# Kernel tuning notes

Measured on AMD Instinct MI355X. Metric: run time of the kernel, lower is better.

The kernel has to match this reference:

```python
import jax, jax.numpy as jnp
import numpy as np

EPS = 1e-5
NUM_GROUPS = 32


def group_norm(x, num_groups=NUM_GROUPS, eps=EPS):
    # x: [B, C, H, W]; normalize over (C//G, H, W) per group, no affine
    B, C, H, W = x.shape
    xg = x.reshape(B, num_groups, C // num_groups, H, W)
    mean = xg.mean(axis=(2, 3, 4), keepdims=True)
    var = xg.var(axis=(2, 3, 4), keepdims=True)
    xg = (xg - mean) * jax.lax.rsqrt(var + eps)
    return xg.reshape(B, C, H, W)


def nin(x, W, b):
    # 1x1 dense projection over channel dim: [B,C,H,W] x [C,O] -> [B,O,H,W]
    return jnp.einsum('bchw,co->bohw', x, W) + b[None, :, None, None]


def setup_inputs() -> dict:
    key = jax.random.key(0)
    ks = jax.random.split(key, 9)
    B, C, H, W_ = 32, 512, 32, 32
    s = 1.0 / np.sqrt(C)
    return {
        'x': jax.random.normal(ks[0], (B, C, H, W_), jnp.float32),
        'Wq': jax.random.normal(ks[1], (C, C), jnp.float32) * s,
        'bq': jnp.zeros((C,), jnp.float32),
        'Wk': jax.random.normal(ks[2], (C, C), jnp.float32) * s,
        'bk': jnp.zeros((C,), jnp.float32),
        'Wv': jax.random.normal(ks[3], (C, C), jnp.float32) * s,
        'bv': jnp.zeros((C,), jnp.float32),
        'Wn': jax.random.normal(ks[4], (C, C), jnp.float32) * (0.05 * s),
        'bn': jnp.zeros((C,), jnp.float32),
    }


def reference(x, Wq, bq, Wk, bk, Wv, bv, Wn, bn):
    B, C, H, W_ = x.shape
    h = group_norm(x)
    q = nin(h, Wq, bq)
    k = nin(h, Wk, bk)
    v = nin(h, Wv, bv)
    scale = jnp.asarray(C, x.dtype) ** -0.5
    # full spatial attention: [B, H, W, H', W']
    w = jnp.einsum('bchw,bcHW->bhwHW', q, k) * scale
    w = w.reshape(B, H, W_, H * W_)
    w = jax.nn.softmax(w, axis=-1)
    w = w.reshape(B, H, W_, H, W_)
    h = jnp.einsum('bhwHW,bcHW->bchw', w, v)
    h = nin(h, Wn, bn)
    return x + h
```

## Files before the change

kernel.cpp:

```cpp
#include <hip/hip_runtime.h>
#include <cstdint>

#define B_   32
#define C_   512
#define N_   1024
#define G_   32
#define CG_  16

typedef unsigned short u16;
typedef unsigned char u8;
typedef unsigned long long u64;

static constexpr float kEps = 1e-5f;
static constexpr float kLog2Scale = 0.06375871752987579f;

using f32x4  = __attribute__((ext_vector_type(4))) float;
using short8 = __attribute__((ext_vector_type(8))) short;
using i64x2  = __attribute__((ext_vector_type(2))) long long;

__device__ __forceinline__ u16 f2bf(float f) {
  uint32_t u = __builtin_bit_cast(uint32_t, f);
  u += 0x7fffu + ((u >> 16) & 1u);
  return (u16)(u >> 16);
}
__device__ __forceinline__ float bf2f(u16 h) {
  return __builtin_bit_cast(float, (uint32_t)h << 16);
}
__device__ __forceinline__ int pk4_fp8(float a, float b, float c, float d) {
  int w = __builtin_amdgcn_cvt_pk_fp8_f32(a, b, 0, false);
  w = __builtin_amdgcn_cvt_pk_fp8_f32(c, d, w, true);
  return w;
}
__device__ __forceinline__ int f8pos(int k) {
  const int c8 = (k >> 3) & 7;
  return (k & ~63) + ((c8 & 3) << 4) + ((c8 >> 2) << 3) + (k & 4);
}

__device__ __forceinline__ void gload16(const void* g, void* lds) {
  __builtin_amdgcn_global_load_lds(
      (__attribute__((address_space(1))) void*)(uintptr_t)g,
      (__attribute__((address_space(3))) void*)(uint32_t)(uintptr_t)lds,
      16, 0, 0);
}

__device__ __forceinline__ uint3 remap_xcd() {
  const int gx = gridDim.x, gy = gridDim.y, gz = gridDim.z;
  const int nwg = gx * gy * gz;
  const int lin = blockIdx.x + gx * (blockIdx.y + gy * blockIdx.z);
  const int q = nwg >> 3, r = nwg & 7;
  const int xcd = lin & 7, pos = lin >> 3;
  int nid = (xcd < r ? xcd * (q + 1) : r * (q + 1) + (xcd - r) * q) + pos;
  uint3 o;
  o.x = nid % gx; nid /= gx;
  o.y = nid % gy; o.z = nid / gy;
  return o;
}

__global__ __launch_bounds__(256) void wcvt_kernel(
    const float* __restrict__ Wq, const float* __restrict__ Wk,
    const float* __restrict__ Wv, u16* __restrict__ Wab, u16* __restrict__ Wbb) {
  const int idx = blockIdx.x * 256 + threadIdx.x;
  const int src = idx >> 16;
  const int e = (idx & 65535) * 4;
  const float* W = (src == 0) ? Wq : (src == 1) ? Wk : Wv;
  u16* D = (src == 0) ? Wab : (src == 1) ? Wbb : (Wab + 262144);
  const float4 v = *(const float4*)(W + e);
  ushort4 st;
  st.x = f2bf(v.x); st.y = f2bf(v.y); st.z = f2bf(v.z); st.w = f2bf(v.w);
  *(ushort4*)(D + e) = st;
}

__global__ __launch_bounds__(256) void wtr_kernel(
    const float* __restrict__ Wn, u16* __restrict__ Wtn) {
  __shared__ float tile[64][65];
  const int c0 = blockIdx.y * 64, o0 = blockIdx.x * 64;
  const int tx = threadIdx.x & 15, ty = threadIdx.x >> 4;
#pragma unroll
  for (int rr = 0; rr < 64; rr += 16) {
    const int c = c0 + ty + rr;
    const float4 v = *(const float4*)(Wn + (size_t)c * 512 + o0 + tx * 4);
    tile[ty + rr][tx * 4 + 0] = v.x;
    tile[ty + rr][tx * 4 + 1] = v.y;
    tile[ty + rr][tx * 4 + 2] = v.z;
    tile[ty + rr][tx * 4 + 3] = v.w;
  }
  __syncthreads();
#pragma unroll
  for (int rr = 0; rr < 64; rr += 16) {
    const int o = o0 + ty + rr;
    ushort4 st;
    st.x = f2bf(tile[tx * 4 + 0][ty + rr]);
    st.y = f2bf(tile[tx * 4 + 1][ty + rr]);
    st.z = f2bf(tile[tx * 4 + 2][ty + rr]);
    st.w = f2bf(tile[tx * 4 + 3][ty + rr]);
    *(ushort4*)(Wtn + (size_t)o * 512 + c0 + tx * 4) = st;
  }
}

__global__ __launch_bounds__(512) void biask_kernel(
    const float* __restrict__ Wk, const float* __restrict__ bq,
    const float* __restrict__ Wn, const float* __restrict__ bv,
    const float* __restrict__ bn, float* __restrict__ wkbq,
    float* __restrict__ bvn) {
  const int t = threadIdx.x;
  if (blockIdx.x == 0) {
    float s = 0.f;
    const float* row = Wk + (size_t)t * 512;
    for (int o = 0; o < 512; ++o) s += row[o] * bq[o];
    wkbq[t] = s;
  } else {
    float s = 0.f;
    for (int c = 0; c < 512; ++c) s += bv[c] * Wn[(size_t)c * 512 + t];
    bvn[t] = s + bn[t];
  }
}

__global__ __launch_bounds__(256) void gn_fused(const float* __restrict__ x,
                                                u8* __restrict__ Hn8,
                                                u8* __restrict__ HnT8) {
  __shared__ u16 lds2[16 * 1032];
  __shared__ float red[10];
  const int bg = blockIdx.x, b = bg >> 5, g = bg & 31;
  const int t = threadIdx.x;
  const float4* p4 = (const float4*)(x + (size_t)bg * 16384);
  float s = 0.f, s2 = 0.f;
  for (int i = t; i < 4096; i += 256) {
    const float4 v = p4[i];
    const int e = i * 4, ic = e >> 10, n = e & 1023;
    ushort4 sv;
    sv.x = f2bf(v.x); sv.y = f2bf(v.y); sv.z = f2bf(v.z); sv.w = f2bf(v.w);
    *(ushort4*)(lds2 + ic * 1032 + n) = sv;
    s  += v.x + v.y + v.z + v.w;
    s2 += v.x * v.x + v.y * v.y + v.z * v.z + v.w * v.w;
  }
#pragma unroll
  for (int o = 32; o; o >>= 1) { s += __shfl_xor(s, o); s2 += __shfl_xor(s2, o); }
  const int lane = t & 63, w = t >> 6;
  if (lane == 0) { red[w] = s; red[4 + w] = s2; }
  __syncthreads();
  if (t == 0) {
    s  = red[0] + red[1] + red[2] + red[3];
    s2 = red[4] + red[5] + red[6] + red[7];
    const float inv = 1.0f / 16384.0f;
    const float mean = s * inv;
    const float var  = s2 * inv - mean * mean;
    red[8] = mean;
    red[9] = rsqrtf(var + kEps);
  }
  __syncthreads();
  const float mean = red[8], rstd = red[9];
#pragma unroll
  for (int r = 0; r < 4; ++r) {
    const int n = t + 256 * r;
    float vals[16];
#pragma unroll
    for (int ic = 0; ic < 16; ++ic)
      vals[ic] = (bf2f(lds2[ic * 1032 + n]) - mean) * rstd;
    const u64 lo = (u64)(uint32_t)pk4_fp8(vals[0], vals[1], vals[2], vals[3]) |
                   ((u64)(uint32_t)pk4_fp8(vals[4], vals[5], vals[6], vals[7]) << 32);
    const u64 hi = (u64)(uint32_t)pk4_fp8(vals[8], vals[9], vals[10], vals[11]) |
                   ((u64)(uint32_t)pk4_fp8(vals[12], vals[13], vals[14], vals[15]) << 32);
    u8* rb = Hn8 + ((size_t)(b * N_ + n)) * C_;
    *(u64*)(rb + f8pos(g * 16))     = lo;
    *(u64*)(rb + f8pos(g * 16 + 8)) = hi;
  }
  const int nb = t * 4;
#pragma unroll
  for (int ic = 0; ic < 16; ++ic) {
    const ushort4 hv = *(const ushort4*)(lds2 + ic * 1032 + nb);
    const int wv = pk4_fp8((bf2f(hv.x) - mean) * rstd, (bf2f(hv.y) - mean) * rstd,
                           (bf2f(hv.z) - mean) * rstd, (bf2f(hv.w) - mean) * rstd);
    *(int*)(HnT8 + ((size_t)(b * C_ + g * 16 + ic)) * N_ + f8pos(nb)) = wv;
  }
}

__global__ __launch_bounds__(256) void gemm_w128(
    const u16* __restrict__ Ab, const u16* __restrict__ Bb, u8* __restrict__ Ob) {
  __shared__ u16 Alds[128 * 64];
  __shared__ u16 Blds[128 * 64];
  const int p = blockIdx.z;
  const u16* A = Ab + (size_t)p * 262144;
  const u16* B = Bb + (size_t)p * 262144;
  u8* O = Ob + (size_t)p * 262144;
  const int m0 = blockIdx.y * 128, n0 = blockIdx.x * 128;
  const int tid = threadIdx.x, lane = tid & 63, wid = tid >> 6;
  const int wm = wid >> 1, wn = wid & 1;
  const int sr = lane >> 3, scb = (lane & 7) ^ sr;
  const u16* Ag = A + (size_t)(m0 + wid * 32 + sr) * 512 + scb * 8;
  const u16* Bg = B + (size_t)(n0 + wid * 32 + sr) * 512 + scb * 8;
  char* Al = (char*)Alds + wid * 4096;
  char* Bl = (char*)Blds + wid * 4096;
  const int arow = lane & 15, g4 = lane >> 4, rx = lane & 7;
  f32x4 acc[4][4] = {};
  for (int k = 0; k < 512; k += 64) {
#pragma unroll
    for (int g = 0; g < 4; ++g) {
      gload16(Ag + k + g * (8 * 512), Al + g * 1024);
      gload16(Bg + k + g * (8 * 512), Bl + g * 1024);
    }
    __syncthreads();
#pragma unroll
    for (int kk = 0; kk < 2; ++kk) {
      const int pc = ((kk * 4 + g4) ^ rx) * 16;
      short8 a[4], b[4];
#pragma unroll
      for (int i = 0; i < 4; ++i)
        a[i] = *(const short8*)((const char*)Alds + (wm * 64 + i * 16 + arow) * 128 + pc);
#pragma unroll
      for (int j = 0; j < 4; ++j)
        b[j] = *(const short8*)((const char*)Blds + (wn * 64 + j * 16 + arow) * 128 + pc);
#pragma unroll
      for (int i = 0; i < 4; ++i)
#pragma unroll
        for (int j = 0; j < 4; ++j)
          acc[i][j] = __builtin_amdgcn_mfma_f32_16x16x32_bf16(a[i], b[j], acc[i][j], 0, 0, 0);
    }
    __syncthreads();
  }
#pragma unroll
  for (int i = 0; i < 4; ++i) {
    const int rowg = m0 + wm * 64 + i * 16 + ((lane >> 4) * 4);
#pragma unroll
    for (int j = 0; j < 4; ++j) {
      const int colg = n0 + wn * 64 + j * 16 + (lane & 15);
      const f32x4 v = acc[i][j];
      *(int*)(O + (size_t)colg * 512 + f8pos(rowg)) =
          pk4_fp8(v[0], v[1], v[2], v[3]);
    }
  }
}

#define LDA8_(D, BASE, MH)                                                      \
  _Pragma("unroll")                                                             \
  for (int i_ = 0; i_ < 4; ++i_) {                                              \
    const int rr_ = wm * 128 + (MH) * 64 + i_ * 16 + arow;                      \
    D[i_] = *(const i64x2*)((BASE) + rr_ * 64 +                                 \
                            ((g4 ^ ((rr_ >> 1) & 3)) << 4));                    \
  }
#define LDB8_(D, BASE)                                                          \
  _Pragma("unroll")                                                             \
  for (int j_ = 0; j_ < 4; ++j_) {                                              \
    const int rr_ = wn * 64 + j_ * 16 + arow;                                   \
    D[j_] = *(const i64x2*)((BASE) + rr_ * 64 +                                 \
                            ((g4 ^ ((rr_ >> 1) & 3)) << 4));                    \
  }
#define MM8_(ACC, AA, BB, H)                                                    \
  __builtin_amdgcn_s_setprio(1);                                                \
  _Pragma("unroll")                                                             \
  for (int i_ = 0; i_ < 4; ++i_)                                                \
    _Pragma("unroll")                                                           \
    for (int j_ = 0; j_ < 4; ++j_)                                              \
      ACC[i_][j_] = __builtin_amdgcn_mfma_f32_16x16x32_fp8_fp8(                 \
          AA[i_][H], BB[j_][H], ACC[i_][j_], 0, 0, 0);                          \
  __builtin_amdgcn_s_setprio(0);

__device__ __forceinline__ void gemm_core256_f8(
    const u8* __restrict__ A, const u8* __restrict__ B,
    int Ktot, int m0, int n0,
    char* Alds, char* Blds, f32x4 acc0[4][4], f32x4 acc1[4][4]) {
  const int tid = threadIdx.x, lane = tid & 63, wid = tid >> 6;
  const int wm = wid >> 2, wn = wid & 3;
  const int rl = lane >> 2;
  const int c16 = (lane & 3) ^ ((lane >> 3) & 3);
  const u8* Ag = A + (size_t)(m0 + wid * 32 + rl) * Ktot + c16 * 16;
  const u8* Bg = B + (size_t)(n0 + wid * 32 + rl) * Ktot + c16 * 16;
  char* Al = Alds + wid * 2048;
  char* Bl = Blds + wid * 2048;
  const long long r16 = (long long)16 * Ktot;
  const int arow = lane & 15, g4 = lane >> 4;
  const int nt = Ktot >> 6;

#pragma unroll
  for (int g = 0; g < 2; ++g) {
    gload16(Ag + g * r16, Al + g * 1024);
    gload16(Bg + g * r16, Bl + g * 1024);
  }
  asm volatile("s_waitcnt vmcnt(0)" ::: "memory");
  __builtin_amdgcn_s_barrier();
  i64x2 aX[4], aY[4], bX[4];
  LDA8_(aX, Alds, 0);

  for (int t = 0; t < nt; ++t) {
    const int cur = t & 1;
    const char* Ab = Alds + cur * 16384;
    const char* Bb = Blds + cur * 16384;
    const char* An = Alds + (cur ^ 1) * 16384;
    char* Aln = Al + (cur ^ 1) * 16384;
    char* Bln = Bl + (cur ^ 1) * 16384;
    const bool nx = (t + 1 < nt);
    const long long ko = (long long)(t + 1) * 64;

    if (nx) {
#pragma unroll
      for (int g = 0; g < 2; ++g) gload16(Bg + ko + g * r16, Bln + g * 1024);
    }
    LDB8_(bX, Bb);
    LDA8_(aY, Ab, 1);
    asm volatile("s_waitcnt lgkmcnt(4)" ::: "memory");
    __builtin_amdgcn_sched_barrier(0);
    __builtin_amdgcn_s_barrier();
    MM8_(acc0, aX, bX, 0);

    if (nx) {
#pragma unroll
      for (int g = 0; g < 2; ++g) gload16(Ag + ko + g * r16, Aln + g * 1024);
    }
    asm volatile("s_waitcnt lgkmcnt(0)" ::: "memory");
    __builtin_amdgcn_sched_barrier(0);
    __builtin_amdgcn_s_barrier();
    MM8_(acc1, aY, bX, 0);

    __builtin_amdgcn_sched_barrier(0);
    __builtin_amdgcn_s_barrier();
    MM8_(acc0, aX, bX, 1);

    if (nx) {
      asm volatile("s_waitcnt vmcnt(0)" ::: "memory");
    }
    __builtin_amdgcn_sched_barrier(0);
    __builtin_amdgcn_s_barrier();
    if (nx) {
      LDA8_(aX, An, 0);
    }
    MM8_(acc1, aY, bX, 1);
  }
}

__device__ __forceinline__ void copy_out_tile(const char* SH, u8* O, int LDC,
                                              int m0, int n0) {
  const int tid = threadIdx.x;
#pragma unroll
  for (int it = 0; it < 8; ++it) {
    const int flat = it * 8192 + tid * 16;
    const int row = flat >> 8, col = flat & 255;
    *(int4*)(O + (size_t)(n0 + row) * LDC + m0 + col) =
        *(const int4*)(SH + row * 256 + (col ^ ((row & 15) << 4)));
  }
}

__global__ __launch_bounds__(512, 2) void gemm_hwq_f8(
    const u8* __restrict__ Wqk8, const u8* __restrict__ Hn8,
    const float* __restrict__ wkbq, u8* __restrict__ HWq8) {
  __shared__ char SH[4 * 256 * 64];
  const uint3 bid = remap_xcd();
  const int z = bid.z;
  const u8* B = Hn8 + (size_t)z * ((size_t)N_ * C_);
  u8* O = HWq8 + (size_t)z * ((size_t)N_ * C_);
  const int m0 = bid.y * 256, n0 = bid.x * 256;
  f32x4 acc0[4][4] = {};
  f32x4 acc1[4][4] = {};
  gemm_core256_f8(Wqk8, B, 512, m0, n0, SH, SH + 32768, acc0, acc1);

  const int lane = threadIdx.x & 63, wid = threadIdx.x >> 6;
  const int wm = wid >> 2, wn = wid & 3;
  __syncthreads();
#pragma unroll
  for (int i = 0; i < 8; ++i) {
    const int ml = wm * 128 + i * 16 + ((lane >> 4) * 4);
    const float4 bv = *(const float4*)(wkbq + m0 + ml);
    const int fp = f8pos(ml);
#pragma unroll
    for (int j = 0; j < 4; ++j) {
      const int nl = wn * 64 + j * 16 + (lane & 15);
      const f32x4 v = (i < 4) ? acc0[i][j] : acc1[i - 4][j];
      *(int*)(SH + nl * 256 + (fp ^ ((nl & 15) << 4))) =
          pk4_fp8(v[0] + bv.x, v[1] + bv.y, v[2] + bv.z, v[3] + bv.w);
    }
  }
  __syncthreads();
  copy_out_tile(SH, O, 512, m0, n0);
}

__global__ __launch_bounds__(512, 2) void gemm_s_f8(
    const u8* __restrict__ Hn8, const u8* __restrict__ HWq8,
    u8* __restrict__ P8, float* __restrict__ Psum) {
  __shared__ char SH[4 * 256 * 64];
  const uint3 bid = remap_xcd();
  const int z = bid.z;
  const u8* A = Hn8  + (size_t)z * ((size_t)N_ * C_);
  const u8* B = HWq8 + (size_t)z * ((size_t)N_ * C_);
  u8*       O = P8   + (size_t)z * ((size_t)N_ * N_);
  const int m0 = bid.y * 256, n0 = bid.x * 256;
  f32x4 acc0[4][4] = {};
  f32x4 acc1[4][4] = {};
  gemm_core256_f8(A, B, 512, m0, n0, SH, SH + 32768, acc0, acc1);

  const int lane = threadIdx.x & 63, wid = threadIdx.x >> 6;
  const int wm = wid >> 2, wn = wid & 3;
  float psum[4] = {0.f, 0.f, 0.f, 0.f};
  __syncthreads();
#pragma unroll
  for (int i = 0; i < 8; ++i) {
    const int ml = wm * 128 + i * 16 + ((lane >> 4) * 4);
    const int fp = f8pos(ml);
#pragma unroll
    for (int j = 0; j < 4; ++j) {
      const int nl = wn * 64 + j * 16 + (lane & 15);
      const f32x4 v = (i < 4) ? acc0[i][j] : acc1[i - 4][j];
      const float p0 = __builtin_exp2f(v[0] * kLog2Scale) * 0.0625f;
      const float p1 = __builtin_exp2f(v[1] * kLog2Scale) * 0.0625f;
      const float p2 = __builtin_exp2f(v[2] * kLog2Scale) * 0.0625f;
      const float p3 = __builtin_exp2f(v[3] * kLog2Scale) * 0.0625f;
      psum[j] += (p0 + p1) + (p2 + p3);
      *(int*)(SH + nl * 256 + (fp ^ ((nl & 15) << 4))) = pk4_fp8(p0, p1, p2, p3);
    }
  }
  const int slot = (m0 >> 7) + wm;
  float* Ps = Psum + ((size_t)z * 8 + slot) * N_;
#pragma unroll
  for (int j = 0; j < 4; ++j) {
    float r = psum[j];
    r += __shfl_xor(r, 16);
    r += __shfl_xor(r, 32);
    if (lane < 16) Ps[n0 + wn * 64 + j * 16 + lane] = r;
  }
  __syncthreads();
  copy_out_tile(SH, O, 1024, m0, n0);
}

__global__ __launch_bounds__(512, 1) void gemm_pvf_f8(
    const u8* __restrict__ HnT8, const u8* __restrict__ P8,
    const float* __restrict__ Psum, const u8* __restrict__ Wvn8,
    const float* __restrict__ x, const float* __restrict__ bvn,
    float* __restrict__ Out) {
  __shared__ char SH[147456];
  char* Abuf = SH;
  char* Bbuf = SH + 65536;
  char* H2   = SH + 81920;
  const uint3 bid = remap_xcd();
  const int z = bid.z;
  const u8* A = HnT8 + (size_t)z * ((size_t)N_ * C_);
  const u8* B = P8   + (size_t)z * ((size_t)N_ * N_);
  const int n0 = bid.x * 128;
  const int tid = threadIdx.x, lane = tid & 63, wid = tid >> 6;
  const int wm = wid >> 1, wn = wid & 1;
  const int rl = lane >> 2;
  const int c16 = (lane & 3) ^ ((lane >> 3) & 3);
  const u8* Ag = A + (size_t)(wid * 64 + rl) * 1024 + c16 * 16;
  const u8* Bg = B + (size_t)(n0 + wid * 16 + rl) * 1024 + c16 * 16;
  const int arow = lane & 15, g4 = lane >> 4;
  f32x4 acc0[4][4] = {};
  f32x4 acc1[4][4] = {};

#pragma unroll
  for (int g = 0; g < 4; ++g)
    gload16(Ag + (size_t)g * (16 * 1024), Abuf + wid * 4096 + g * 1024);
  gload16(Bg, Bbuf + wid * 1024);
  asm volatile("s_waitcnt vmcnt(0)" ::: "memory");
  __builtin_amdgcn_s_barrier();
  i64x2 aX[4], aY[4], bX[4];
  LDA8_(aX, Abuf, 0);

  for (int t = 0; t < 16; ++t) {
    const int cur = t & 1;
    const char* Ab = Abuf + cur * 32768;
    const char* Bb = Bbuf + cur * 8192;
    const char* An = Abuf + (cur ^ 1) * 32768;
    const bool nx = (t + 1 < 16);
    const long long ko = (long long)(t + 1) * 64;

    if (nx) gload16(Bg + ko, Bbuf + (cur ^ 1) * 8192 + wid * 1024);
    LDB8_(bX, Bb);
    LDA8_(aY, Ab, 1);
    asm volatile("s_waitcnt lgkmcnt(4)" ::: "memory");
    __builtin_amdgcn_sched_barrier(0);
    __builtin_amdgcn_s_barrier();
    MM8_(acc0, aX, bX, 0);

    if (nx) {
#pragma unroll
      for (int g = 0; g < 4; ++g)
        gload16(Ag + ko + (size_t)g * (16 * 1024),
                Abuf + (cur ^ 1) * 32768 + wid * 4096 + g * 1024);
    }
    asm volatile("s_waitcnt lgkmcnt(0)" ::: "memory");
    __builtin_amdgcn_sched_barrier(0);
    __builtin_amdgcn_s_barrier();
    MM8_(acc1, aY, bX, 0);

    __builtin_amdgcn_sched_barrier(0);
    __builtin_amdgcn_s_barrier();
    MM8_(acc0, aX, bX, 1);

    if (nx) {
      asm volatile("s_waitcnt vmcnt(0)" ::: "memory");
    }
    __builtin_amdgcn_sched_barrier(0);
    __builtin_amdgcn_s_barrier();
    if (nx) {
      LDA8_(aX, An, 0);
    }
    MM8_(acc1, aY, bX, 1);
  }

  const float* Ps = Psum + (size_t)z * 8 * N_;
  float inv[4];
#pragma unroll
  for (int j = 0; j < 4; ++j) {
    const int ng = n0 + wn * 64 + j * 16 + (lane & 15);
    float s = 0.f;
#pragma unroll
    for (int k = 0; k < 8; ++k) s += Ps[k * N_ + ng];
    inv[j] = 1.0f / s;
  }
#pragma unroll
  for (int i = 0; i < 8; ++i) {
    const int c = wm * 128 + i * 16 + ((lane >> 4) * 4);
    const int fp = f8pos(c);
    const int ck = fp >> 4, sub = fp & 15;
#pragma unroll
    for (int j = 0; j < 4; ++j) {
      const int nl = wn * 64 + j * 16 + (lane & 15);
      const f32x4 v = (i < 4) ? acc0[i][j] : acc1[i - 4][j];
      *(int*)(H2 + nl * 512 + ((ck ^ (nl & 15)) << 4) + sub) =
          pk4_fp8(v[0] * inv[j], v[1] * inv[j], v[2] * inv[j], v[3] * inv[j]);
    }
  }
  __syncthreads();

  const int wmf = wid >> 2, wnf = wid & 3;
  f32x4 acc2[4][8] = {};
#pragma unroll
  for (int t = 0; t < 8; ++t) {
    i64x2 a2[4], b2[8];
#pragma unroll
    for (int i = 0; i < 4; ++i) {
      const int rn = wmf * 64 + i * 16 + arow;
      a2[i] = *(const i64x2*)(H2 + rn * 512 + (((t * 4 + g4) ^ (rn & 15)) << 4));
    }
#pragma unroll
    for (int j = 0; j < 8; ++j) {
      const int ro = wnf * 128 + j * 16 + arow;
      b2[j] = *(const i64x2*)(Wvn8 + (size_t)ro * 512 + t * 64 + g4 * 16);
    }
#pragma unroll
    for (int i = 0; i < 4; ++i)
#pragma unroll
      for (int j = 0; j < 8; ++j)
        acc2[i][j] = __builtin_amdgcn_mfma_f32_16x16x32_fp8_fp8(
            a2[i][0], b2[j][0], acc2[i][j], 0, 0, 0);
#pragma unroll
    for (int i = 0; i < 4; ++i)
#pragma unroll
      for (int j = 0; j < 8; ++j)
        acc2[i][j] = __builtin_amdgcn_mfma_f32_16x16x32_fp8_fp8(
            a2[i][1], b2[j][1], acc2[i][j], 0, 0, 0);
  }

  const float* xb = x + (size_t)z * ((size_t)C_ * N_);
  float* Ob = Out + (size_t)z * ((size_t)C_ * N_);
#pragma unroll
  for (int i = 0; i < 4; ++i) {
    const int rown = n0 + wmf * 64 + i * 16 + ((lane >> 4) * 4);
#pragma unroll
    for (int j = 0; j < 8; ++j) {
      const int colo = wnf * 128 + j * 16 + (lane & 15);
      const float bc = bvn[colo];
      const size_t off = (size_t)colo * N_ + rown;
      const float4 xv = *(const float4*)(xb + off);
      const f32x4 v = acc2[i][j];
      float4 ov;
      ov.x = xv.x + v[0] + bc;
      ov.y = xv.y + v[1] + bc;
      ov.z = xv.z + v[2] + bc;
      ov.w = xv.w + v[3] + bc;
      *(float4*)(Ob + off) = ov;
    }
  }
}

__global__ void sentinel_kernel(float* out, int n, float v) {
  const int i = blockIdx.x * blockDim.x + threadIdx.x;
  if (i < n) out[i] = v;
}

extern "C" void kernel_launch(void* const* d_in, const int* in_sizes, int n_in,
                              void* d_out, int out_size, void* d_ws, size_t ws_size,
                              hipStream_t stream) {
  const float* x  = (const float*)d_in[0];
  const float* Wq = (const float*)d_in[1];
  const float* bq = (const float*)d_in[2];
  const float* Wk = (const float*)d_in[3];
  const float* Wv = (const float*)d_in[5];
  const float* bv = (const float*)d_in[6];
  const float* Wn = (const float*)d_in[7];
  const float* bn = (const float*)d_in[8];
  float* out = (float*)d_out;

  char* ws = (char*)d_ws;
  size_t off = 0;
  u16* Wab = (u16*)(ws + off); off += (size_t)2 * 262144 * 2;
  u16* Wbb = (u16*)(ws + off); off += (size_t)2 * 262144 * 2;
  u8*  W8  = (u8*)(ws + off);  off += (size_t)2 * 262144;
  float* wkbq = (float*)(ws + off); off += 512 * 4;
  float* bvn  = (float*)(ws + off); off += 512 * 4;
  const size_t bnc = (size_t)B_ * N_ * C_;
  u8* Hn8  = (u8*)(ws + off); off += bnc;
  u8* HnT8 = (u8*)(ws + off); off += bnc;
  u8* HWq8 = (u8*)(ws + off); off += bnc;
  u8* P8   = (u8*)(ws + off); off += (size_t)B_ * N_ * N_;
  float* Psum = (float*)(ws + off); off += (size_t)B_ * 8 * N_ * 4;

  if (ws_size < off) {
    const float v = 1.0e6f + (float)(ws_size >> 20);
    sentinel_kernel<<<(out_size + 255) / 256, 256, 0, stream>>>(out, out_size, v);
    return;
  }

  wcvt_kernel<<<768, 256, 0, stream>>>(Wq, Wk, Wv, Wab, Wbb);
  wtr_kernel<<<dim3(8, 8), 256, 0, stream>>>(Wn, Wbb + 262144);
  biask_kernel<<<2, 512, 0, stream>>>(Wk, bq, Wn, bv, bn, wkbq, bvn);
  gn_fused<<<B_ * G_, 256, 0, stream>>>(x, Hn8, HnT8);
  gemm_w128<<<dim3(4, 4, 2), 256, 0, stream>>>(Wab, Wbb, W8);
  gemm_hwq_f8<<<dim3(4, 2, B_), 512, 0, stream>>>(W8, Hn8, wkbq, HWq8);
  gemm_s_f8<<<dim3(4, 4, B_), 512, 0, stream>>>(Hn8, HWq8, P8, Psum);
  gemm_pvf_f8<<<dim3(8, 1, B_), 512, 0, stream>>>(HnT8, P8, Psum, W8 + 262144, x, bvn, out);
}
```

Measured before the change: 192.2 us.

## Halve PV tile width in fused PV+output kernel to double grid and occupancy

Shrinks the gemm_pvf_f8 column tile from 128 to 64 query positions, doubling the grid to 512 blocks. LDS drops from 144KB to 72KB by aliasing the H2 staging buffer onto the A buffer (with an added barrier), and launch bounds allow more blocks per CU. Only four waves now load the smaller B tile. The aim is better CU fill and latency hiding, at the cost of re-reading the full HnT8 panel and Wvn weights twice as often per batch.

```diff
diff --git a/kernel.cpp b/kernel.cpp
--- a/kernel.cpp
+++ b/kernel.cpp
@@ -244,12 +244,28 @@
     D[j_] = *(const i64x2*)((BASE) + rr_ * 64 +                                 \
                             ((g4 ^ ((rr_ >> 1) & 3)) << 4));                    \
   }
+#define LDB8J2_(D, BASE)                                                        \
+  _Pragma("unroll")                                                             \
+  for (int j_ = 0; j_ < 2; ++j_) {                                              \
+    const int rr_ = wn * 32 + j_ * 16 + arow;                                   \
+    D[j_] = *(const i64x2*)((BASE) + rr_ * 64 +                                 \
+                            ((g4 ^ ((rr_ >> 1) & 3)) << 4));                    \
+  }
 #define MM8_(ACC, AA, BB, H)                                                    \
   __builtin_amdgcn_s_setprio(1);                                                \
   _Pragma("unroll")                                                             \
   for (int i_ = 0; i_ < 4; ++i_)                                                \
     _Pragma("unroll")                                                           \
     for (int j_ = 0; j_ < 4; ++j_)                                              \
+      ACC[i_][j_] = __builtin_amdgcn_mfma_f32_16x16x32_fp8_fp8(                 \
+          AA[i_][H], BB[j_][H], ACC[i_][j_], 0, 0, 0);                          \
+  __builtin_amdgcn_s_setprio(0);
+#define MM8J2_(ACC, AA, BB, H)                                                  \
+  __builtin_amdgcn_s_setprio(1);                                                \
+  _Pragma("unroll")                                                             \
+  for (int i_ = 0; i_ < 4; ++i_)                                                \
+    _Pragma("unroll")                                                           \
+    for (int j_ = 0; j_ < 2; ++j_)                                              \
       ACC[i_][j_] = __builtin_amdgcn_mfma_f32_16x16x32_fp8_fp8(                 \
           AA[i_][H], BB[j_][H], ACC[i_][j_], 0, 0, 0);                          \
   __builtin_amdgcn_s_setprio(0);
@@ -418,20 +434,20 @@
   copy_out_tile(SH, O, 1024, m0, n0);
 }
 
-__global__ __launch_bounds__(512, 1) void gemm_pvf_f8(
+__global__ __launch_bounds__(512, 4) void gemm_pvf_f8(
     const u8* __restrict__ HnT8, const u8* __restrict__ P8,
     const float* __restrict__ Psum, const u8* __restrict__ Wvn8,
     const float* __restrict__ x, const float* __restrict__ bvn,
     float* __restrict__ Out) {
-  __shared__ char SH[147456];
+  __shared__ char SH[73728];
   char* Abuf = SH;
   char* Bbuf = SH + 65536;
-  char* H2   = SH + 81920;
+  char* H2   = SH;
   const uint3 bid = remap_xcd();
   const int z = bid.z;
   const u8* A = HnT8 + (size_t)z * ((size_t)N_ * C_);
   const u8* B = P8   + (size_t)z * ((size_t)N_ * N_);
-  const int n0 = bid.x * 128;
+  const int n0 = bid.x * 64;
   const int tid = threadIdx.x, lane = tid & 63, wid = tid >> 6;
   const int wm = wid >> 1, wn = wid & 1;
   const int rl = lane >> 2;
@@ -439,33 +455,33 @@
   const u8* Ag = A + (size_t)(wid * 64 + rl) * 1024 + c16 * 16;
   const u8* Bg = B + (size_t)(n0 + wid * 16 + rl) * 1024 + c16 * 16;
   const int arow = lane & 15, g4 = lane >> 4;
-  f32x4 acc0[4][4] = {};
-  f32x4 acc1[4][4] = {};
+  f32x4 acc0[4][2] = {};
+  f32x4 acc1[4][2] = {};
 
 #pragma unroll
   for (int g = 0; g < 4; ++g)
     gload16(Ag + (size_t)g * (16 * 1024), Abuf + wid * 4096 + g * 1024);
-  gload16(Bg, Bbuf + wid * 1024);
+  if (wid < 4) gload16(Bg, Bbuf + wid * 1024);
   asm volatile("s_waitcnt vmcnt(0)" ::: "memory");
   __builtin_amdgcn_s_barrier();
-  i64x2 aX[4], aY[4], bX[4];
+  i64x2 aX[4], aY[4], bX[2];
   LDA8_(aX, Abuf, 0);
 
   for (int t = 0; t < 16; ++t) {
     const int cur = t & 1;
     const char* Ab = Abuf + cur * 32768;
-    const char* Bb = Bbuf + cur * 8192;
+    const char* Bb = Bbuf + cur * 4096;
     const char* An = Abuf + (cur ^ 1) * 32768;
     const bool nx = (t + 1 < 16);
     const long long ko = (long long)(t + 1) * 64;
 
-    if (nx) gload16(Bg + ko, Bbuf + (cur ^ 1) * 8192 + wid * 1024);
-    LDB8_(bX, Bb);
+    if (nx && wid < 4) gload16(Bg + ko, Bbuf + (cur ^ 1) * 4096 + wid * 1024);
+    LDB8J2_(bX, Bb);
     LDA8_(aY, Ab, 1);
     asm volatile("s_waitcnt lgkmcnt(4)" ::: "memory");
     __builtin_amdgcn_sched_barrier(0);
     __builtin_amdgcn_s_barrier();
-    MM8_(acc0, aX, bX, 0);
+    MM8J2_(acc0, aX, bX, 0);
 
     if (nx) {
 #pragma unroll
@@ -476,11 +492,11 @@
     asm volatile("s_waitcnt lgkmcnt(0)" ::: "memory");
     __builtin_amdgcn_sched_barrier(0);
     __builtin_amdgcn_s_barrier();
-    MM8_(acc1, aY, bX, 0);
-
-    __builtin_amdgcn_sched_barrier(0);
-    __builtin_amdgcn_s_barrier();
-    MM8_(acc0, aX, bX, 1);
+    MM8J2_(acc1, aY, bX, 0);
+
+    __builtin_amdgcn_sched_barrier(0);
+    __builtin_amdgcn_s_barrier();
+    MM8J2_(acc0, aX, bX, 1);
 
     if (nx) {
       asm volatile("s_waitcnt vmcnt(0)" ::: "memory");
@@ -490,14 +506,15 @@
     if (nx) {
       LDA8_(aX, An, 0);
     }
-    MM8_(acc1, aY, bX, 1);
-  }
+    MM8J2_(acc1, aY, bX, 1);
+  }
+  __syncthreads();
 
   const float* Ps = Psum + (size_t)z * 8 * N_;
-  float inv[4];
-#pragma unroll
-  for (int j = 0; j < 4; ++j) {
-    const int ng = n0 + wn * 64 + j * 16 + (lane & 15);
+  float inv[2];
+#pragma unroll
+  for (int j = 0; j < 2; ++j) {
+    const int ng = n0 + wn * 32 + j * 16 + (lane & 15);
     float s = 0.f;
 #pragma unroll
     for (int k = 0; k < 8; ++k) s += Ps[k * N_ + ng];
@@ -509,8 +526,8 @@
     const int fp = f8pos(c);
     const int ck = fp >> 4, sub = fp & 15;
 #pragma unroll
-    for (int j = 0; j < 4; ++j) {
-      const int nl = wn * 64 + j * 16 + (lane & 15);
+    for (int j = 0; j < 2; ++j) {
+      const int nl = wn * 32 + j * 16 + (lane & 15);
       const f32x4 v = (i < 4) ? acc0[i][j] : acc1[i - 4][j];
       *(int*)(H2 + nl * 512 + ((ck ^ (nl & 15)) << 4) + sub) =
           pk4_fp8(v[0] * inv[j], v[1] * inv[j], v[2] * inv[j], v[3] * inv[j]);
@@ -519,13 +536,13 @@
   __syncthreads();
 
   const int wmf = wid >> 2, wnf = wid & 3;
-  f32x4 acc2[4][8] = {};
+  f32x4 acc2[2][8] = {};
 #pragma unroll
   for (int t = 0; t < 8; ++t) {
-    i64x2 a2[4], b2[8];
-#pragma unroll
-    for (int i = 0; i < 4; ++i) {
-      const int rn = wmf * 64 + i * 16 + arow;
+    i64x2 a2[2], b2[8];
+#pragma unroll
+    for (int i = 0; i < 2; ++i) {
+      const int rn = wmf * 32 + i * 16 + arow;
       a2[i] = *(const i64x2*)(H2 + rn * 512 + (((t * 4 + g4) ^ (rn & 15)) << 4));
     }
 #pragma unroll
@@ -534,13 +551,13 @@
       b2[j] = *(const i64x2*)(Wvn8 + (size_t)ro * 512 + t * 64 + g4 * 16);
     }
 #pragma unroll
-    for (int i = 0; i < 4; ++i)
+    for (int i = 0; i < 2; ++i)
 #pragma unroll
       for (int j = 0; j < 8; ++j)
         acc2[i][j] = __builtin_amdgcn_mfma_f32_16x16x32_fp8_fp8(
             a2[i][0], b2[j][0], acc2[i][j], 0, 0, 0);
 #pragma unroll
-    for (int i = 0; i < 4; ++i)
+    for (int i = 0; i < 2; ++i)
 #pragma unroll
       for (int j = 0; j < 8; ++j)
         acc2[i][j] = __builtin_amdgcn_mfma_f32_16x16x32_fp8_fp8(
@@ -550,8 +567,8 @@
   const float* xb = x + (size_t)z * ((size_t)C_ * N_);
   float* Ob = Out + (size_t)z * ((size_t)C_ * N_);
 #pragma unroll
-  for (int i = 0; i < 4; ++i) {
-    const int rown = n0 + wmf * 64 + i * 16 + ((lane >> 4) * 4);
+  for (int i = 0; i < 2; ++i) {
+    const int rown = n0 + wmf * 32 + i * 16 + ((lane >> 4) * 4);
 #pragma unroll
     for (int j = 0; j < 8; ++j) {
       const int colo = wnf * 128 + j * 16 + (lane & 15);
@@ -614,5 +631,5 @@
   gemm_w128<<<dim3(4, 4, 2), 256, 0, stream>>>(Wab, Wbb, W8);
   gemm_hwq_f8<<<dim3(4, 2, B_), 512, 0, stream>>>(W8, Hn8, wkbq, HWq8);
   gemm_s_f8<<<dim3(4, 4, B_), 512, 0, stream>>>(Hn8, HWq8, P8, Psum);
-  gemm_pvf_f8<<<dim3(8, 1, B_), 512, 0, stream>>>(HnT8, P8, Psum, W8 + 262144, x, bvn, out);
-}
+  gemm_pvf_f8<<<dim3(16, 1, B_), 512, 0, stream>>>(HnT8, P8, Psum, W8 + 262144, x, bvn, out);
+}
```

New measurement: 235.9 us. +22.8%, slower.
